# Kernel optimization log

Measured on AMD Instinct MI355X. Metric: run time of the kernel, lower is better.

## Reference

```python
import jax, jax.numpy as jnp
import numpy as np

N_AGENTS = 32
STATE_DIM = 512
LATENT = 16
H = 64  # attention_hidden_dim
N1 = N_AGENTS
N2 = N_AGENTS * (N_AGENTS - 1) // 2
NF = N1 + N2
B = 32768
# pairwise indices, same order as itertools.combinations(range(n), 2)
_PI, _PJ = np.triu_indices(N_AGENTS, k=1)
PI = jnp.asarray(_PI)
PJ = jnp.asarray(_PJ)


def setup_inputs() -> dict:
    key = jax.random.key(0)
    ks = jax.random.split(key, 24)
    s = 0.1  # small init scale (xavier gain 0.5)
    inp = {
        "agent_q_values": jax.random.normal(ks[0], (B, N_AGENTS), jnp.float32),
        "state": jax.random.normal(ks[1], (B, STATE_DIM), jnp.float32),
        "agent_semantics": jax.random.normal(ks[2], (B, N_AGENTS, LATENT), jnp.float32),
        # order-1 shape functions, stacked over N1 functions, weights in [in,out] layout
        "w1_1": jax.random.normal(ks[3], (N1, 1, 8), jnp.float32) * s,
        "b1_1": jnp.zeros((N1, 8), jnp.float32),
        "w2_1": jax.random.normal(ks[4], (N1, 8, 4), jnp.float32) * s,
        "b2_1": jnp.zeros((N1, 4), jnp.float32),
        "w3_1": jax.random.normal(ks[5], (N1, 4, 1), jnp.float32) * s,
        "b3_1": jnp.zeros((N1, 1), jnp.float32),
        # order-2 shape functions, stacked over N2 pairs
        "w1_2": jax.random.normal(ks[6], (N2, 2, 8), jnp.float32) * s,
        "b1_2": jnp.zeros((N2, 8), jnp.float32),
        "w2_2": jax.random.normal(ks[7], (N2, 8, 4), jnp.float32) * s,
        "b2_2": jnp.zeros((N2, 4), jnp.float32),
        "w3_2": jax.random.normal(ks[8], (N2, 4, 1), jnp.float32) * s,
        "b3_2": jnp.zeros((N2, 1), jnp.float32),
        # state encoder
        "ws_w": jax.random.normal(ks[9], (STATE_DIM, H), jnp.float32) * (1.0 / np.sqrt(STATE_DIM)),
        "ws_b": jnp.zeros((H,), jnp.float32),
        # semantic encoder
        "wz_w": jax.random.normal(ks[10], (LATENT * N_AGENTS, H), jnp.float32) * (1.0 / np.sqrt(LATENT * N_AGENTS)),
        "wz_b": jnp.zeros((H,), jnp.float32),
        # attention net
        "wa1_w": jax.random.normal(ks[11], (2 * H, H), jnp.float32) * (1.0 / np.sqrt(2 * H)),
        "wa1_b": jnp.zeros((H,), jnp.float32),
        "wa2_w": jax.random.normal(ks[12], (H, NF), jnp.float32) * (1.0 / np.sqrt(H)),
        "wa2_b": jnp.zeros((NF,), jnp.float32),
        # bias net
        "wb1_w": jax.random.normal(ks[13], (STATE_DIM, H), jnp.float32) * (1.0 / np.sqrt(STATE_DIM)),
        "wb1_b": jnp.zeros((H,), jnp.float32),
        "wb2_w": jax.random.normal(ks[14], (H, 1), jnp.float32) * (1.0 / np.sqrt(H)),
        "wb2_b": jnp.zeros((1,), jnp.float32),
    }
    return inp


def _shape_fns(x, w1, b1, w2, b2, w3, b3):
    # x: [B, N, D_in]; weights stacked over N functions; abs() on weights (monotonicity)
    h = jax.nn.elu(jnp.einsum("bnd,ndh->bnh", x, jnp.abs(w1)) + b1)   # [B,N,8]
    h = jax.nn.elu(jnp.einsum("bnh,nhk->bnk", h, jnp.abs(w2)) + b2)   # [B,N,4]
    f = jnp.einsum("bnk,nk->bn", h, jnp.abs(w3)[:, :, 0]) + b3[:, 0]  # [B,N]
    return f


def reference(agent_q_values, state, agent_semantics,
              w1_1, b1_1, w2_1, b2_1, w3_1, b3_1,
              w1_2, b1_2, w2_2, b2_2, w3_2, b3_2,
              ws_w, ws_b, wz_w, wz_b,
              wa1_w, wa1_b, wa2_w, wa2_b,
              wb1_w, wb1_b, wb2_w, wb2_b):
    q = agent_q_values  # [B, n_agents]
    # order-1 shape functions: input is scalar Q_i
    f1 = _shape_fns(q[:, :, None], w1_1, b1_1, w2_1, b2_1, w3_1, b3_1)   # [B, N1]
    # order-2 shape functions: input is [Q_i, Q_j] per pair
    q_pairs = jnp.stack([q[:, PI], q[:, PJ]], axis=-1)                    # [B, N2, 2]
    f2 = _shape_fns(q_pairs, w1_2, b1_2, w2_2, b2_2, w3_2, b3_2)          # [B, N2]
    shape_outputs = jnp.concatenate([f1, f2], axis=-1)                    # [B, NF]

    state_enc = jax.nn.relu(state @ ws_w + ws_b)                          # [B, H]
    sem_flat = agent_semantics.reshape(agent_semantics.shape[0], -1)      # [B, n*latent]
    sem_enc = jax.nn.relu(sem_flat @ wz_w + wz_b)                         # [B, H]
    combined = jnp.concatenate([state_enc, sem_enc], axis=-1)             # [B, 2H]
    logits = jax.nn.relu(combined @ wa1_w + wa1_b) @ wa2_w + wa2_b        # [B, NF]
    attention_weights = jax.nn.softmax(logits, axis=-1)

    weighted_sum = jnp.sum(attention_weights * shape_outputs, axis=-1, keepdims=True)
    bias = jax.nn.relu(state @ wb1_w + wb1_b) @ wb2_w + wb2_b             # [B, 1]
    q_total = weighted_sum + bias
    return (q_total, attention_weights, shape_outputs)
```

## Files before the change

### kernel.cpp

```cpp
#include <hip/hip_runtime.h>
#include <cstdint>
#include <cstddef>

#define NAG 32
#define N1C 32
#define N2C 496
#define NF 528
#define HD 64
#define SD 512

typedef __attribute__((ext_vector_type(8))) short bf16x8;
typedef __attribute__((ext_vector_type(4))) float f32x4;
#define MFMA16(a, b, c) __builtin_amdgcn_mfma_f32_16x16x32_bf16(a, b, c, 0, 0, 0)

__device__ __forceinline__ unsigned short f2bf(float f) {
    unsigned int u = __float_as_uint(f);
    u += 0x7fffu + ((u >> 16) & 1u);
    return (unsigned short)(u >> 16);
}
__device__ __forceinline__ unsigned int pack2(float a, float b) {
    return (unsigned int)f2bf(a) | ((unsigned int)f2bf(b) << 16);
}
__device__ __forceinline__ float elu_f(float x) {
    return x > 0.f ? x : (__expf(x) - 1.f);
}

#define OFF_WST   0
#define OFF_WB1T  32768
#define OFF_WZT   65536
#define OFF_WA1T  98304
#define OFF_WA2T  106496
#define PREP_TOT  140288

__global__ __launch_bounds__(256) void prep_kernel(
    const float* __restrict__ ws_w, const float* __restrict__ wb1_w,
    const float* __restrict__ wz_w, const float* __restrict__ wa1_w,
    const float* __restrict__ wa2_w, unsigned short* __restrict__ ws)
{
    int i = blockIdx.x * 256 + threadIdx.x;
    if (i >= PREP_TOT) return;
    float v;
    if (i < OFF_WB1T) {
        int j = i - OFF_WST; int n = j >> 9, k = j & 511;
        v = ws_w[k * 64 + n];
    } else if (i < OFF_WZT) {
        int j = i - OFF_WB1T; int n = j >> 9, k = j & 511;
        v = wb1_w[k * 64 + n];
    } else if (i < OFF_WA1T) {
        int j = i - OFF_WZT; int n = j >> 9, k = j & 511;
        v = wz_w[k * 64 + n];
    } else if (i < OFF_WA2T) {
        int j = i - OFF_WA1T; int n = j >> 7, k = j & 127;
        v = wa1_w[k * 64 + n];
    } else {
        int j = i - OFF_WA2T; int n = j >> 6, k = j & 63;
        v = wa2_w[k * NF + n];
    }
    ws[i] = f2bf(v);
}

#define SROWS 64
__global__ __launch_bounds__(576) void shape_kernel(
    const float* __restrict__ q,
    const float* __restrict__ w1_1, const float* __restrict__ b1_1,
    const float* __restrict__ w2_1, const float* __restrict__ b2_1,
    const float* __restrict__ w3_1, const float* __restrict__ b3_1,
    const float* __restrict__ w1_2, const float* __restrict__ b1_2,
    const float* __restrict__ w2_2, const float* __restrict__ b2_2,
    const float* __restrict__ w3_2, const float* __restrict__ b3_2,
    float* __restrict__ shape_out, int B)
{
    __shared__ float qs[SROWS][NAG];

    int tid = threadIdx.x;
    int f = tid;
    bool valid = f < NF;
    int fe = valid ? f : (NF - 1);

    float w1a[8], w1b[8], b1v[8], w2v[32], b2v[4], w3v[4], b3v;
    int pi, pj;
    if (fe < N1C) {
        int n = fe;
        pi = n; pj = n;
        #pragma unroll
        for (int k = 0; k < 8; k++) { w1a[k] = fabsf(w1_1[n*8+k]); w1b[k] = 0.f; b1v[k] = b1_1[n*8+k]; }
        #pragma unroll
        for (int t = 0; t < 32; t++) w2v[t] = fabsf(w2_1[n*32+t]);
        #pragma unroll
        for (int j = 0; j < 4; j++) { b2v[j] = b2_1[n*4+j]; w3v[j] = fabsf(w3_1[n*4+j]); }
        b3v = b3_1[n];
    } else {
        int n = fe - N1C;
        int p = n, i = 0, c = NAG - 1;
        while (p >= c) { p -= c; c--; i++; }
        pi = i; pj = i + 1 + p;
        #pragma unroll
        for (int k = 0; k < 8; k++) { w1a[k] = fabsf(w1_2[n*16+k]); w1b[k] = fabsf(w1_2[n*16+8+k]); b1v[k] = b1_2[n*8+k]; }
        #pragma unroll
        for (int t = 0; t < 32; t++) w2v[t] = fabsf(w2_2[n*32+t]);
        #pragma unroll
        for (int j = 0; j < 4; j++) { b2v[j] = b2_2[n*4+j]; w3v[j] = fabsf(w3_2[n*4+j]); }
        b3v = b3_2[n];
    }

    int row0 = blockIdx.x * SROWS;
    if (tid < 512) {
        float4 v = *(const float4*)&q[(size_t)row0 * NAG + tid * 4];
        *(float4*)&((float*)qs)[tid * 4] = v;
    }
    __syncthreads();

    #pragma unroll 4
    for (int rr = 0; rr < SROWS; rr++) {
        float qi = qs[rr][pi];
        float qj = qs[rr][pj];
        float h1[8];
        #pragma unroll
        for (int k = 0; k < 8; k++) h1[k] = elu_f(w1a[k]*qi + w1b[k]*qj + b1v[k]);
        float h2[4];
        #pragma unroll
        for (int j = 0; j < 4; j++) {
            float a = b2v[j];
            #pragma unroll
            for (int k = 0; k < 8; k++) a += h1[k] * w2v[k*4 + j];
            h2[j] = elu_f(a);
        }
        float fv = b3v;
        #pragma unroll
        for (int j = 0; j < 4; j++) fv += h2[j] * w3v[j];
        if (valid) shape_out[(size_t)(row0 + rr) * NF + f] = fv;
    }
}

#define RB 64
__global__ __launch_bounds__(256, 2) void enc_mfma(
    const float* __restrict__ state,
    const float* __restrict__ sem,
    const unsigned short* __restrict__ wsbuf,
    const float* __restrict__ ws_b, const float* __restrict__ wz_b,
    const float* __restrict__ wa1_b, const float* __restrict__ wa2_b,
    const float* __restrict__ wb1_b, const float* __restrict__ wb2_w,
    const float* __restrict__ wb2_b,
    const float* __restrict__ shape_out,
    float* __restrict__ q_total,
    float* __restrict__ attn_out)
{
    __shared__ unsigned short sA[RB][72];
    __shared__ unsigned short sComb[RB][136];
    __shared__ unsigned short sH[RB][72];

    const unsigned short* wsT  = wsbuf + OFF_WST;
    const unsigned short* wb1T = wsbuf + OFF_WB1T;
    const unsigned short* wzT  = wsbuf + OFF_WZT;
    const unsigned short* wa1T = wsbuf + OFF_WA1T;
    const unsigned short* wa2T = wsbuf + OFF_WA2T;

    int tid  = threadIdx.x;
    int lane = tid & 63;
    int w    = tid >> 6;
    int col  = lane & 15;
    int quad = lane >> 4;
    int r0   = blockIdx.x * RB;
    int rowt = w * 16;

    f32x4 accS[4], accB[4], accZ[4];
    #pragma unroll
    for (int ct = 0; ct < 4; ct++) {
        accS[ct] = (f32x4){0.f,0.f,0.f,0.f};
        accB[ct] = (f32x4){0.f,0.f,0.f,0.f};
        accZ[ct] = (f32x4){0.f,0.f,0.f,0.f};
    }

    for (int chunk = 0; chunk < 8; chunk++) {
        __syncthreads();
        #pragma unroll
        for (int i = 0; i < 4; i++) {
            int idx = i * 256 + tid;
            int sr = idx >> 4;
            int sc = (idx & 15) << 2;
            float4 v = *(const float4*)&state[(size_t)(r0 + sr) * SD + chunk * 64 + sc];
            uint2 p; p.x = pack2(v.x, v.y); p.y = pack2(v.z, v.w);
            *(uint2*)&sA[sr][sc] = p;
        }
        __syncthreads();
        #pragma unroll
        for (int ks = 0; ks < 2; ks++) {
            bf16x8 a = *(const bf16x8*)&sA[rowt + col][ks * 32 + quad * 8];
            int wof = chunk * 64 + ks * 32 + quad * 8;
            #pragma unroll
            for (int ct = 0; ct < 4; ct++) {
                bf16x8 bS = *(const bf16x8*)&wsT [(ct * 16 + col) * SD + wof];
                bf16x8 bB = *(const bf16x8*)&wb1T[(ct * 16 + col) * SD + wof];
                accS[ct] = MFMA16(a, bS, accS[ct]);
                accB[ct] = MFMA16(a, bB, accB[ct]);
            }
        }
    }

    for (int chunk = 0; chunk < 8; chunk++) {
        __syncthreads();
        #pragma unroll
        for (int i = 0; i < 4; i++) {
            int idx = i * 256 + tid;
            int sr = idx >> 4;
            int sc = (idx & 15) << 2;
            float4 v = *(const float4*)&sem[(size_t)(r0 + sr) * SD + chunk * 64 + sc];
            uint2 p; p.x = pack2(v.x, v.y); p.y = pack2(v.z, v.w);
            *(uint2*)&sA[sr][sc] = p;
        }
        __syncthreads();
        #pragma unroll
        for (int ks = 0; ks < 2; ks++) {
            bf16x8 a = *(const bf16x8*)&sA[rowt + col][ks * 32 + quad * 8];
            int wof = chunk * 64 + ks * 32 + quad * 8;
            #pragma unroll
            for (int ct = 0; ct < 4; ct++) {
                bf16x8 bZ = *(const bf16x8*)&wzT[(ct * 16 + col) * SD + wof];
                accZ[ct] = MFMA16(a, bZ, accZ[ct]);
            }
        }
    }

    #pragma unroll
    for (int ct = 0; ct < 4; ct++) {
        float bs = ws_b[ct * 16 + col];
        float bz = wz_b[ct * 16 + col];
        #pragma unroll
        for (int reg = 0; reg < 4; reg++) {
            int rr = rowt + quad * 4 + reg;
            sComb[rr][ct * 16 + col]      = f2bf(fmaxf(accS[ct][reg] + bs, 0.f));
            sComb[rr][64 + ct * 16 + col] = f2bf(fmaxf(accZ[ct][reg] + bz, 0.f));
        }
    }

    float qbv[4];
    #pragma unroll
    for (int reg = 0; reg < 4; reg++) {
        float p = 0.f;
        #pragma unroll
        for (int ct = 0; ct < 4; ct++)
            p += fmaxf(accB[ct][reg] + wb1_b[ct * 16 + col], 0.f) * wb2_w[ct * 16 + col];
        #pragma unroll
        for (int m = 1; m < 16; m <<= 1) p += __shfl_xor(p, m, 64);
        qbv[reg] = p;
    }

    f32x4 accH[4];
    #pragma unroll
    for (int ct = 0; ct < 4; ct++) accH[ct] = (f32x4){0.f,0.f,0.f,0.f};
    #pragma unroll
    for (int ks = 0; ks < 4; ks++) {
        bf16x8 a = *(const bf16x8*)&sComb[rowt + col][ks * 32 + quad * 8];
        #pragma unroll
        for (int ct = 0; ct < 4; ct++) {
            bf16x8 b = *(const bf16x8*)&wa1T[(ct * 16 + col) * 128 + ks * 32 + quad * 8];
            accH[ct] = MFMA16(a, b, accH[ct]);
        }
    }
    #pragma unroll
    for (int ct = 0; ct < 4; ct++) {
        float bh = wa1_b[ct * 16 + col];
        #pragma unroll
        for (int reg = 0; reg < 4; reg++)
            sH[rowt + quad * 4 + reg][ct * 16 + col] = f2bf(fmaxf(accH[ct][reg] + bh, 0.f));
    }

    bf16x8 ha0 = *(const bf16x8*)&sH[rowt + col][quad * 8];
    bf16x8 ha1 = *(const bf16x8*)&sH[rowt + col][32 + quad * 8];

    float sAcc[4] = {0.f,0.f,0.f,0.f};
    float wAcc[4] = {0.f,0.f,0.f,0.f};
    for (int nt = 0; nt < 33; nt++) {
        f32x4 acc = (f32x4){0.f,0.f,0.f,0.f};
        const unsigned short* wp = &wa2T[(nt * 16 + col) * 64 + quad * 8];
        acc = MFMA16(ha0, *(const bf16x8*)wp, acc);
        acc = MFMA16(ha1, *(const bf16x8*)(wp + 32), acc);
        float lb = wa2_b[nt * 16 + col];
        #pragma unroll
        for (int reg = 0; reg < 4; reg++) {
            float e = __expf(acc[reg] + lb);
            sAcc[reg] += e;
            wAcc[reg] += e * shape_out[(size_t)(r0 + rowt + quad * 4 + reg) * NF + nt * 16 + col];
        }
    }
    float inv[4];
    #pragma unroll
    for (int reg = 0; reg < 4; reg++) {
        float s = sAcc[reg], ww = wAcc[reg];
        #pragma unroll
        for (int m = 1; m < 16; m <<= 1) { s += __shfl_xor(s, m, 64); ww += __shfl_xor(ww, m, 64); }
        inv[reg] = 1.f / s;
        if (col == 0)
            q_total[r0 + rowt + quad * 4 + reg] = ww * inv[reg] + qbv[reg] + wb2_b[0];
    }

    for (int nt = 0; nt < 33; nt++) {
        f32x4 acc = (f32x4){0.f,0.f,0.f,0.f};
        const unsigned short* wp = &wa2T[(nt * 16 + col) * 64 + quad * 8];
        acc = MFMA16(ha0, *(const bf16x8*)wp, acc);
        acc = MFMA16(ha1, *(const bf16x8*)(wp + 32), acc);
        float lb = wa2_b[nt * 16 + col];
        #pragma unroll
        for (int reg = 0; reg < 4; reg++) {
            float e = __expf(acc[reg] + lb);
            attn_out[(size_t)(r0 + rowt + quad * 4 + reg) * NF + nt * 16 + col] = e * inv[reg];
        }
    }
}

extern "C" void kernel_launch(void* const* d_in, const int* in_sizes, int n_in,
                              void* d_out, int out_size, void* d_ws, size_t ws_size,
                              hipStream_t stream) {
    const float* q     = (const float*)d_in[0];
    const float* state = (const float*)d_in[1];
    const float* sem   = (const float*)d_in[2];
    const float* w1_1  = (const float*)d_in[3];
    const float* b1_1  = (const float*)d_in[4];
    const float* w2_1  = (const float*)d_in[5];
    const float* b2_1  = (const float*)d_in[6];
    const float* w3_1  = (const float*)d_in[7];
    const float* b3_1  = (const float*)d_in[8];
    const float* w1_2  = (const float*)d_in[9];
    const float* b1_2  = (const float*)d_in[10];
    const float* w2_2  = (const float*)d_in[11];
    const float* b2_2  = (const float*)d_in[12];
    const float* w3_2  = (const float*)d_in[13];
    const float* b3_2  = (const float*)d_in[14];
    const float* ws_w  = (const float*)d_in[15];
    const float* ws_b  = (const float*)d_in[16];
    const float* wz_w  = (const float*)d_in[17];
    const float* wz_b  = (const float*)d_in[18];
    const float* wa1_w = (const float*)d_in[19];
    const float* wa1_b = (const float*)d_in[20];
    const float* wa2_w = (const float*)d_in[21];
    const float* wa2_b = (const float*)d_in[22];
    const float* wb1_w = (const float*)d_in[23];
    const float* wb1_b = (const float*)d_in[24];
    const float* wb2_w = (const float*)d_in[25];
    const float* wb2_b = (const float*)d_in[26];

    int B = in_sizes[0] / NAG;

    float* out_q    = (float*)d_out;
    float* out_attn = out_q + B;
    float* out_shp  = out_attn + (size_t)B * NF;

    unsigned short* wsbuf = (unsigned short*)d_ws;

    prep_kernel<<<(PREP_TOT + 255) / 256, 256, 0, stream>>>(
        ws_w, wb1_w, wz_w, wa1_w, wa2_w, wsbuf);

    shape_kernel<<<B / SROWS, 576, 0, stream>>>(q,
        w1_1, b1_1, w2_1, b2_1, w3_1, b3_1,
        w1_2, b1_2, w2_2, b2_2, w3_2, b3_2,
        out_shp, B);

    enc_mfma<<<B / RB, 256, 0, stream>>>(state, sem, wsbuf,
        ws_b, wz_b, wa1_b, wa2_b, wb1_b, wb2_w, wb2_b,
        out_shp, out_q, out_attn);
}
```

Baseline: 407.1 us.

## Load MFMA A-operands directly from global memory, removing LDS staging and barriers

The encoder GEMM no longer stages state and semantic rows through shared memory. Each lane now loads its own 8 fp32 values per k-step straight from global memory, packs them to bf16 in registers, and the state and semantic loops are fused into one 16-step loop. This removes the per-chunk __syncthreads pairs and the LDS round trip, and adds two barriers after the sComb/sH writes. The cost is strided, less coalesced global loads: each lane reads 32 bytes from a different row, and latency hiding now depends only on unroll 2.

Result: slower. 419.1 us (+3.0%).

```diff
diff --git a/kernel.cpp b/kernel.cpp
--- a/kernel.cpp
+++ b/kernel.cpp
@@ -145,7 +145,6 @@
     float* __restrict__ q_total,
     float* __restrict__ attn_out)
 {
-    __shared__ unsigned short sA[RB][72];
     __shared__ unsigned short sComb[RB][136];
     __shared__ unsigned short sH[RB][72];
 
@@ -163,6 +162,12 @@
     int r0   = blockIdx.x * RB;
     int rowt = w * 16;
 
+    const float* __restrict__ srowS = state + (size_t)(r0 + rowt + col) * SD + quad * 8;
+    const float* __restrict__ srowZ = sem   + (size_t)(r0 + rowt + col) * SD + quad * 8;
+    const unsigned short* __restrict__ bS0 = wsT  + col * SD + quad * 8;
+    const unsigned short* __restrict__ bB0 = wb1T + col * SD + quad * 8;
+    const unsigned short* __restrict__ bZ0 = wzT  + col * SD + quad * 8;
+
     f32x4 accS[4], accB[4], accZ[4];
     #pragma unroll
     for (int ct = 0; ct < 4; ct++) {
@@ -171,53 +176,30 @@
         accZ[ct] = (f32x4){0.f,0.f,0.f,0.f};
     }
 
-    for (int chunk = 0; chunk < 8; chunk++) {
-        __syncthreads();
-        #pragma unroll
-        for (int i = 0; i < 4; i++) {
-            int idx = i * 256 + tid;
-            int sr = idx >> 4;
-            int sc = (idx & 15) << 2;
-            float4 v = *(const float4*)&state[(size_t)(r0 + sr) * SD + chunk * 64 + sc];
-            uint2 p; p.x = pack2(v.x, v.y); p.y = pack2(v.z, v.w);
-            *(uint2*)&sA[sr][sc] = p;
-        }
-        __syncthreads();
-        #pragma unroll
-        for (int ks = 0; ks < 2; ks++) {
-            bf16x8 a = *(const bf16x8*)&sA[rowt + col][ks * 32 + quad * 8];
-            int wof = chunk * 64 + ks * 32 + quad * 8;
-            #pragma unroll
-            for (int ct = 0; ct < 4; ct++) {
-                bf16x8 bS = *(const bf16x8*)&wsT [(ct * 16 + col) * SD + wof];
-                bf16x8 bB = *(const bf16x8*)&wb1T[(ct * 16 + col) * SD + wof];
-                accS[ct] = MFMA16(a, bS, accS[ct]);
-                accB[ct] = MFMA16(a, bB, accB[ct]);
-            }
-        }
-    }
-
-    for (int chunk = 0; chunk < 8; chunk++) {
-        __syncthreads();
-        #pragma unroll
-        for (int i = 0; i < 4; i++) {
-            int idx = i * 256 + tid;
-            int sr = idx >> 4;
-            int sc = (idx & 15) << 2;
-            float4 v = *(const float4*)&sem[(size_t)(r0 + sr) * SD + chunk * 64 + sc];
-            uint2 p; p.x = pack2(v.x, v.y); p.y = pack2(v.z, v.w);
-            *(uint2*)&sA[sr][sc] = p;
-        }
-        __syncthreads();
-        #pragma unroll
-        for (int ks = 0; ks < 2; ks++) {
-            bf16x8 a = *(const bf16x8*)&sA[rowt + col][ks * 32 + quad * 8];
-            int wof = chunk * 64 + ks * 32 + quad * 8;
-            #pragma unroll
-            for (int ct = 0; ct < 4; ct++) {
-                bf16x8 bZ = *(const bf16x8*)&wzT[(ct * 16 + col) * SD + wof];
-                accZ[ct] = MFMA16(a, bZ, accZ[ct]);
-            }
+    #pragma unroll 2
+    for (int ks = 0; ks < 16; ks++) {
+        float4 s0 = *(const float4*)(srowS + ks * 32);
+        float4 s1 = *(const float4*)(srowS + ks * 32 + 4);
+        float4 z0 = *(const float4*)(srowZ + ks * 32);
+        float4 z1 = *(const float4*)(srowZ + ks * 32 + 4);
+        bf16x8 as, az;
+        {
+            unsigned int* p = (unsigned int*)&as;
+            p[0] = pack2(s0.x, s0.y); p[1] = pack2(s0.z, s0.w);
+            p[2] = pack2(s1.x, s1.y); p[3] = pack2(s1.z, s1.w);
+            unsigned int* pz = (unsigned int*)&az;
+            pz[0] = pack2(z0.x, z0.y); pz[1] = pack2(z0.z, z0.w);
+            pz[2] = pack2(z1.x, z1.y); pz[3] = pack2(z1.z, z1.w);
+        }
+        int wof = ks * 32;
+        #pragma unroll
+        for (int ct = 0; ct < 4; ct++) {
+            bf16x8 bS = *(const bf16x8*)(bS0 + ct * 16 * SD + wof);
+            bf16x8 bB = *(const bf16x8*)(bB0 + ct * 16 * SD + wof);
+            bf16x8 bZ = *(const bf16x8*)(bZ0 + ct * 16 * SD + wof);
+            accS[ct] = MFMA16(as, bS, accS[ct]);
+            accB[ct] = MFMA16(as, bB, accB[ct]);
+            accZ[ct] = MFMA16(az, bZ, accZ[ct]);
         }
     }
 
@@ -232,6 +214,7 @@
             sComb[rr][64 + ct * 16 + col] = f2bf(fmaxf(accZ[ct][reg] + bz, 0.f));
         }
     }
+    __syncthreads();
 
     float qbv[4];
     #pragma unroll
@@ -264,6 +247,7 @@
         for (int reg = 0; reg < 4; reg++)
             sH[rowt + quad * 4 + reg][ct * 16 + col] = f2bf(fmaxf(accH[ct][reg] + bh, 0.f));
     }
+    __syncthreads();
 
     bf16x8 ha0 = *(const bf16x8*)&sH[rowt + col][quad * 8];
     bf16x8 ha1 = *(const bf16x8*)&sH[rowt + col][32 + quad * 8];
```

## Stage per-wave private A tiles in 256-wide K chunks without block barriers

Applied to the files above, without the earlier changes.

Each wave now loads and converts only its own 16 rows of state/semantics into shared memory, in two 256-column halves instead of eight 64-column chunks. Because a wave reads back only the rows it wrote, the two __syncthreads per chunk are removed. Each load batch also issues more float4 reads, giving more memory-level parallelism per wave. The cost is a larger shared A buffer (64x264 shorts), which may reduce occupancy, and higher register pressure from holding eight float4 values in flight.

After: 405.3 us. No clear change (-0.4%).

```diff
diff --git a/kernel.cpp b/kernel.cpp
--- a/kernel.cpp
+++ b/kernel.cpp
@@ -133,6 +133,9 @@
 }
 
 #define RB 64
+#define KH 256
+#define SAP 264
+
 __global__ __launch_bounds__(256, 2) void enc_mfma(
     const float* __restrict__ state,
     const float* __restrict__ sem,
@@ -145,7 +148,7 @@
     float* __restrict__ q_total,
     float* __restrict__ attn_out)
 {
-    __shared__ unsigned short sA[RB][72];
+    __shared__ unsigned short sA[RB][SAP];
     __shared__ unsigned short sComb[RB][136];
     __shared__ unsigned short sH[RB][72];
 
@@ -163,6 +166,10 @@
     int r0   = blockIdx.x * RB;
     int rowt = w * 16;
 
+    const unsigned short* bS0 = wsT  + col * SD + quad * 8;
+    const unsigned short* bB0 = wb1T + col * SD + quad * 8;
+    const unsigned short* bZ0 = wzT  + col * SD + quad * 8;
+
     f32x4 accS[4], accB[4], accZ[4];
     #pragma unroll
     for (int ct = 0; ct < 4; ct++) {
@@ -171,51 +178,57 @@
         accZ[ct] = (f32x4){0.f,0.f,0.f,0.f};
     }
 
-    for (int chunk = 0; chunk < 8; chunk++) {
-        __syncthreads();
-        #pragma unroll
-        for (int i = 0; i < 4; i++) {
-            int idx = i * 256 + tid;
-            int sr = idx >> 4;
-            int sc = (idx & 15) << 2;
-            float4 v = *(const float4*)&state[(size_t)(r0 + sr) * SD + chunk * 64 + sc];
-            uint2 p; p.x = pack2(v.x, v.y); p.y = pack2(v.z, v.w);
-            *(uint2*)&sA[sr][sc] = p;
-        }
-        __syncthreads();
-        #pragma unroll
-        for (int ks = 0; ks < 2; ks++) {
+    #pragma unroll 1
+    for (int h = 0; h < 2; h++) {
+        int c0 = h * KH;
+        #pragma unroll
+        for (int b = 0; b < 2; b++) {
+            float4 v[8];
+            #pragma unroll
+            for (int i = 0; i < 8; i++)
+                v[i] = *(const float4*)&state[(size_t)(r0 + rowt + b*8 + i) * SD + c0 + lane * 4];
+            #pragma unroll
+            for (int i = 0; i < 8; i++) {
+                uint2 p; p.x = pack2(v[i].x, v[i].y); p.y = pack2(v[i].z, v[i].w);
+                *(uint2*)&sA[rowt + b*8 + i][lane * 4] = p;
+            }
+        }
+        #pragma unroll
+        for (int ks = 0; ks < 8; ks++) {
             bf16x8 a = *(const bf16x8*)&sA[rowt + col][ks * 32 + quad * 8];
-            int wof = chunk * 64 + ks * 32 + quad * 8;
+            int wof = c0 + ks * 32;
             #pragma unroll
             for (int ct = 0; ct < 4; ct++) {
-                bf16x8 bS = *(const bf16x8*)&wsT [(ct * 16 + col) * SD + wof];
-                bf16x8 bB = *(const bf16x8*)&wb1T[(ct * 16 + col) * SD + wof];
+                bf16x8 bS = *(const bf16x8*)(bS0 + ct * 16 * SD + wof);
+                bf16x8 bB = *(const bf16x8*)(bB0 + ct * 16 * SD + wof);
                 accS[ct] = MFMA16(a, bS, accS[ct]);
                 accB[ct] = MFMA16(a, bB, accB[ct]);
             }
         }
     }
 
-    for (int chunk = 0; chunk < 8; chunk++) {
-        __syncthreads();
-        #pragma unroll
-        for (int i = 0; i < 4; i++) {
-            int idx = i * 256 + tid;
-            int sr = idx >> 4;
-            int sc = (idx & 15) << 2;
-            float4 v = *(const float4*)&sem[(size_t)(r0 + sr) * SD + chunk * 64 + sc];
-            uint2 p; p.x = pack2(v.x, v.y); p.y = pack2(v.z, v.w);
-            *(uint2*)&sA[sr][sc] = p;
-        }
-        __syncthreads();
-        #pragma unroll
-        for (int ks = 0; ks < 2; ks++) {
+    #pragma unroll 1
+    for (int h = 0; h < 2; h++) {
+        int c0 = h * KH;
+        #pragma unroll
+        for (int b = 0; b < 2; b++) {
+            float4 v[8];
+            #pragma unroll
+            for (int i = 0; i < 8; i++)
+                v[i] = *(const float4*)&sem[(size_t)(r0 + rowt + b*8 + i) * SD + c0 + lane * 4];
+            #pragma unroll
+            for (int i = 0; i < 8; i++) {
+                uint2 p; p.x = pack2(v[i].x, v[i].y); p.y = pack2(v[i].z, v[i].w);
+                *(uint2*)&sA[rowt + b*8 + i][lane * 4] = p;
+            }
+        }
+        #pragma unroll
+        for (int ks = 0; ks < 8; ks++) {
             bf16x8 a = *(const bf16x8*)&sA[rowt + col][ks * 32 + quad * 8];
-            int wof = chunk * 64 + ks * 32 + quad * 8;
+            int wof = c0 + ks * 32;
             #pragma unroll
             for (int ct = 0; ct < 4; ct++) {
-                bf16x8 bZ = *(const bf16x8*)&wzT[(ct * 16 + col) * SD + wof];
+                bf16x8 bZ = *(const bf16x8*)(bZ0 + ct * 16 * SD + wof);
                 accZ[ct] = MFMA16(a, bZ, accZ[ct]);
             }
         }
```
